# Performance work log

Hardware: AMD Instinct MI355X
Metric: run time of the kernel (lower is better)

Reference implementation:

```python
import jax, jax.numpy as jnp
import numpy as np

NUM_HEADS = 8
KEY_DIM = 256
EPS = 1e-16


def setup_inputs() -> dict:
    key = jax.random.key(0)
    k1, k2, k3, k4 = jax.random.split(key, 4)
    b, n, d, m = 2, 20000, 256, 320000
    q = jax.random.normal(k1, (b, n, d), dtype=jnp.float32)
    k = jax.random.normal(k2, (b, n, d), dtype=jnp.float32)
    e = jax.random.randint(k3, (2, m), 0, n, dtype=jnp.int64)
    r = jax.random.randint(k4, (m,), 0, n, dtype=jnp.int64)
    return {"q": q, "k": k, "e": e, "r": r}


def reference(q, k, e, r):
    b, n, d = q.shape
    m = e.shape[1]
    dh = d // NUM_HEADS
    # gather edge endpoints, multiply, sum within each head's d_head chunk
    # (scatter_sum over dim with h=[i//dh] == reshape + sum over last axis)
    src_q = q[:, e[0], :]                      # (b, m, d)
    dst_k = k[:, e[1], :]                      # (b, m, d)
    a = (src_q * dst_k).reshape(b, m, NUM_HEADS, dh).sum(-1)  # (b, m, H)
    a = a / jnp.sqrt(jnp.asarray(KEY_DIM, a.dtype))
    # segment softmax over edges grouped by r (global max subtraction, as in source)
    a = a - a.max()
    ex = jnp.exp(a)                            # (b, m, H)
    seg = jax.ops.segment_sum(ex.transpose(1, 0, 2), r, num_segments=n)  # (n, b, H)
    denom = seg[r].transpose(1, 0, 2)          # (b, m, H)
    return ex / (denom + EPS)
```

## Files before the change

kernel.cpp:

```cpp
#include <hip/hip_runtime.h>
#include <hip/hip_bf16.h>
#include <cmath>

#define D 256
#define NH 8
#define B 2
#define EPW 4
#define SSH 5
#define NBKMAX 1024
#define NCHMAX 512
#define SBLK 1024

#if defined(__has_builtin)
#  if __has_builtin(__builtin_amdgcn_fdot2_f32_bf16)
#    define USE_BF16_DOT 1
#  else
#    define USE_BF16_DOT 0
#  endif
#else
#  define USE_BF16_DOT 0
#endif

#if USE_BF16_DOT
typedef __bf16 bf16x2 __attribute__((ext_vector_type(2)));
#endif

__device__ inline unsigned short f2bf(float f) {
    unsigned u = __float_as_uint(f);
    unsigned r = u + 0x7FFFu + ((u >> 16) & 1u);
    return (unsigned short)(r >> 16);
}

__device__ inline float dot16(const uint4& a, const uint4& b) {
    float p = 0.f;
#if USE_BF16_DOT
    const bf16x2* av = (const bf16x2*)&a;
    const bf16x2* bv = (const bf16x2*)&b;
    #pragma unroll
    for (int w = 0; w < 4; ++w)
        p = __builtin_amdgcn_fdot2_f32_bf16(av[w], bv[w], p, false);
#else
    const unsigned* aw = (const unsigned*)&a;
    const unsigned* bw = (const unsigned*)&b;
    #pragma unroll
    for (int w = 0; w < 4; ++w) {
        float al = __uint_as_float(aw[w] << 16);
        float ah = __uint_as_float(aw[w] & 0xFFFF0000u);
        float bl = __uint_as_float(bw[w] << 16);
        float bh = __uint_as_float(bw[w] & 0xFFFF0000u);
        p = fmaf(al, bl, p);
        p = fmaf(ah, bh, p);
    }
#endif
    return p;
}

__global__ __launch_bounds__(256) void k_conv(
    const float* __restrict__ q, const float* __restrict__ k,
    uint4* __restrict__ qc, uint4* __restrict__ kc,
    float* __restrict__ seg, int segN, int n)
{
    int tid    = blockIdx.x * blockDim.x + threadIdx.x;
    int stride = gridDim.x * blockDim.x;
    for (int i = tid; i < segN; i += stride) seg[i] = 0.f;
    int total = n * B * 32;
    for (int i = tid; i < total; i += stride) {
        int c   = i & 31;
        int row = i >> 5;
        int bb  = (row >= n) ? 1 : 0;
        int node = row - bb * n;
        const float4* qs = (const float4*)(q + ((size_t)row << 8)) + (c << 1);
        const float4* ks = (const float4*)(k + ((size_t)row << 8)) + (c << 1);
        float4 a0 = qs[0], a1 = qs[1];
        float4 b0 = ks[0], b1 = ks[1];
        uint4 pa, pb;
        pa.x = (unsigned)f2bf(a0.x) | ((unsigned)f2bf(a0.y) << 16);
        pa.y = (unsigned)f2bf(a0.z) | ((unsigned)f2bf(a0.w) << 16);
        pa.z = (unsigned)f2bf(a1.x) | ((unsigned)f2bf(a1.y) << 16);
        pa.w = (unsigned)f2bf(a1.z) | ((unsigned)f2bf(a1.w) << 16);
        pb.x = (unsigned)f2bf(b0.x) | ((unsigned)f2bf(b0.y) << 16);
        pb.y = (unsigned)f2bf(b0.z) | ((unsigned)f2bf(b0.w) << 16);
        pb.z = (unsigned)f2bf(b1.x) | ((unsigned)f2bf(b1.y) << 16);
        pb.w = (unsigned)f2bf(b1.z) | ((unsigned)f2bf(b1.w) << 16);
        size_t dst = ((size_t)node * B + bb) * 32 + c;
        qc[dst] = pa;
        kc[dst] = pb;
    }
}


__global__ __launch_bounds__(256) void k_hist2(
    const int* __restrict__ e, int* __restrict__ bh, int m, int nbk)
{
    __shared__ int lh[NBKMAX];
    int b = blockIdx.x;
    int start = b * SBLK, end = min(m, start + SBLK);
    for (int t = threadIdx.x; t < nbk; t += 256) lh[t] = 0;
    __syncthreads();
    for (int j = start + threadIdx.x; j < end; j += 256)
        atomicAdd(&lh[e[j] >> SSH], 1);
    __syncthreads();
    for (int t = threadIdx.x; t < nbk; t += 256)
        bh[(size_t)b * nbk + t] = lh[t];
}

__global__ __launch_bounds__(NCHMAX) void k_colscan(
    int* __restrict__ bh, int* __restrict__ tot, int nch, int nbk)
{
    __shared__ int tmp[NCHMAX];
    int t = blockIdx.x;
    int b = threadIdx.x;
    int v = (b < nch) ? bh[(size_t)b * nbk + t] : 0;
    tmp[b] = v;
    __syncthreads();
    for (int off = 1; off < NCHMAX; off <<= 1) {
        int u = (b >= off) ? tmp[b - off] : 0;
        __syncthreads();
        tmp[b] += u;
        __syncthreads();
    }
    if (b < nch) bh[(size_t)b * nbk + t] = tmp[b] - v;
    if (b == NCHMAX - 1) tot[t] = tmp[b];
}

__global__ __launch_bounds__(256) void k_scatter2(
    const int* __restrict__ e, const int* __restrict__ r,
    const int* __restrict__ bh, const int* __restrict__ tot,
    int4* __restrict__ perm, int m, int nbk)
{
    __shared__ int tl[NBKMAX];
    __shared__ int tp[256];
    int b = blockIdx.x;
    int tid = threadIdx.x;
    for (int i = tid; i < NBKMAX; i += 256)
        tl[i] = (i < nbk) ? tot[i] : 0;
    __syncthreads();
    int s0 = tl[tid * 4 + 0], s1 = tl[tid * 4 + 1];
    int s2 = tl[tid * 4 + 2], s3 = tl[tid * 4 + 3];
    tl[tid * 4 + 0] = 0;
    tl[tid * 4 + 1] = s0;
    tl[tid * 4 + 2] = s0 + s1;
    tl[tid * 4 + 3] = s0 + s1 + s2;
    int v = s0 + s1 + s2 + s3;
    tp[tid] = v;
    __syncthreads();
    for (int off = 1; off < 256; off <<= 1) {
        int u = (tid >= off) ? tp[tid - off] : 0;
        __syncthreads();
        tp[tid] += u;
        __syncthreads();
    }
    int stripbase = tp[tid] - v;
    #pragma unroll
    for (int j2 = 0; j2 < 4; ++j2) tl[tid * 4 + j2] += stripbase;
    __syncthreads();
    __shared__ int cur[NBKMAX];
    for (int t = tid; t < nbk; t += 256)
        cur[t] = bh[(size_t)b * nbk + t] + tl[t];
    __syncthreads();
    int start = b * SBLK, end = min(m, start + SBLK);
    for (int j = start + tid; j < end; j += 256) {
        int e0 = e[j], e1 = e[m + j];
        int pos = atomicAdd(&cur[e0 >> SSH], 1);
        perm[pos] = make_int4(e0, e1, r[j], j);
    }
}

__global__ __launch_bounds__(256) void k_scores_perm(
    const ushort* __restrict__ qc, const ushort* __restrict__ kc,
    const int4* __restrict__ perm,
    float* __restrict__ s, float* __restrict__ seg, int m, int do_swz)
{
    int bid = blockIdx.x;
    if (do_swz) {
        int nb8 = gridDim.x >> 3;
        bid = (bid & 7) * nb8 + (bid >> 3);
    }
    int wave = (bid << 2) + (threadIdx.x >> 6);
    int lane = threadIdx.x & 63;
    int j0 = wave * EPW;
    if (j0 >= m) return;

    int rr[EPW], jo[EPW];
    uint4 qa[EPW], kb[EPW];
    #pragma unroll
    for (int t = 0; t < EPW; ++t) {
        int j = j0 + t;
        int4 p = (j < m) ? perm[j] : make_int4(0, 0, 0, -1);
        rr[t] = p.z;
        jo[t] = p.w;
        qa[t] = ((const uint4*)(qc + (size_t)p.x * (B * D)))[lane];
        kb[t] = ((const uint4*)(kc + (size_t)p.y * (B * D)))[lane];
    }
    __builtin_amdgcn_sched_barrier(0);

    #pragma unroll
    for (int t = 0; t < EPW; ++t) {
        float p = dot16(qa[t], kb[t]);
        p += __shfl_xor(p, 1);
        p += __shfl_xor(p, 2);
        float ex = __expf(p * 0.0625f);
        if ((lane & 3) == 0 && jo[t] >= 0) {
            int bb = lane >> 5;
            int h  = (lane >> 2) & 7;
            s[((size_t)bb * m + jo[t]) * NH + h] = ex;
            atomicAdd(&seg[((size_t)rr[t] * B + bb) * NH + h], ex);
        }
    }
}

__global__ __launch_bounds__(256) void k_scores_fused(
    const ushort* __restrict__ qc, const ushort* __restrict__ kc,
    const int* __restrict__ e, const int* __restrict__ r,
    float* __restrict__ s, float* __restrict__ seg, int m)
{
    int wave = (int)((blockIdx.x * blockDim.x + threadIdx.x) >> 6);
    int lane = threadIdx.x & 63;
    int j0 = wave * EPW;
    if (j0 >= m) return;

    int e0[EPW], e1[EPW], rr[EPW];
    #pragma unroll
    for (int t = 0; t < EPW; ++t) {
        int j = j0 + t;
        int ok = (j < m);
        e0[t] = ok ? e[j]     : 0;
        e1[t] = ok ? e[m + j] : 0;
        rr[t] = ok ? r[j]     : 0;
    }
    uint4 qa[EPW], kb[EPW];
    #pragma unroll
    for (int t = 0; t < EPW; ++t) {
        qa[t] = ((const uint4*)(qc + (size_t)e0[t] * (B * D)))[lane];
        kb[t] = ((const uint4*)(kc + (size_t)e1[t] * (B * D)))[lane];
    }
    __builtin_amdgcn_sched_barrier(0);
    #pragma unroll
    for (int t = 0; t < EPW; ++t) {
        float p = dot16(qa[t], kb[t]);
        p += __shfl_xor(p, 1);
        p += __shfl_xor(p, 2);
        float ex = __expf(p * 0.0625f);
        if ((lane & 3) == 0 && (j0 + t) < m) {
            int bb = lane >> 5;
            int h  = (lane >> 2) & 7;
            s[((size_t)bb * m + (j0 + t)) * NH + h] = ex;
            atomicAdd(&seg[((size_t)rr[t] * B + bb) * NH + h], ex);
        }
    }
}

__global__ __launch_bounds__(256) void k_scores_fused_f32(
    const float* __restrict__ q, const float* __restrict__ k,
    const int* __restrict__ e, const int* __restrict__ r,
    float* __restrict__ s, float* __restrict__ seg, int n, int m)
{
    int wave = (int)((blockIdx.x * blockDim.x + threadIdx.x) >> 6);
    int lane = threadIdx.x & 63;
    int j0 = wave * EPW;
    if (j0 >= m) return;
    int e0[EPW], e1[EPW], rr[EPW];
    #pragma unroll
    for (int t = 0; t < EPW; ++t) {
        int j = j0 + t; int ok = (j < m);
        e0[t] = ok ? e[j] : 0; e1[t] = ok ? e[m + j] : 0; rr[t] = ok ? r[j] : 0;
    }
    float4 qa[B][EPW], kb[B][EPW];
    #pragma unroll
    for (int bb = 0; bb < B; ++bb)
        #pragma unroll
        for (int t = 0; t < EPW; ++t) {
            qa[bb][t] = ((const float4*)(q + ((size_t)bb * n + e0[t]) * D))[lane];
            kb[bb][t] = ((const float4*)(k + ((size_t)bb * n + e1[t]) * D))[lane];
        }
    #pragma unroll
    for (int bb = 0; bb < B; ++bb)
        #pragma unroll
        for (int t = 0; t < EPW; ++t) {
            float4 A = qa[bb][t], K4 = kb[bb][t];
            float p = A.x * K4.x + A.y * K4.y + A.z * K4.z + A.w * K4.w;
            p += __shfl_xor(p, 1); p += __shfl_xor(p, 2); p += __shfl_xor(p, 4);
            float ex = __expf(p * 0.0625f);
            if ((lane & 7) == 0 && (j0 + t) < m) {
                int h = lane >> 3;
                s[((size_t)bb * m + (j0 + t)) * NH + h] = ex;
                atomicAdd(&seg[((size_t)rr[t] * B + bb) * NH + h], ex);
            }
        }
}

__global__ __launch_bounds__(256) void k_norm(
    float* __restrict__ s, const int* __restrict__ r,
    const float* __restrict__ seg, int m)
{
    int i = blockIdx.x * blockDim.x + threadIdx.x;
    int total = B * m;
    if (i >= total) return;
    int bb = (i >= m) ? 1 : 0;
    int j  = i - bb * m;
    const float4* sg = (const float4*)(seg + ((size_t)r[j] * B + bb) * NH);
    float4* sp = (float4*)(s + (size_t)i * NH);
    float4 d0 = sg[0], d1 = sg[1];
    float4 x0 = sp[0], x1 = sp[1];
    x0.x = __fdividef(x0.x, d0.x + 1e-16f);
    x0.y = __fdividef(x0.y, d0.y + 1e-16f);
    x0.z = __fdividef(x0.z, d0.z + 1e-16f);
    x0.w = __fdividef(x0.w, d0.w + 1e-16f);
    x1.x = __fdividef(x1.x, d1.x + 1e-16f);
    x1.y = __fdividef(x1.y, d1.y + 1e-16f);
    x1.z = __fdividef(x1.z, d1.z + 1e-16f);
    x1.w = __fdividef(x1.w, d1.w + 1e-16f);
    sp[0] = x0; sp[1] = x1;
}

extern "C" void kernel_launch(void* const* d_in, const int* in_sizes, int n_in,
                              void* d_out, int out_size, void* d_ws, size_t ws_size,
                              hipStream_t stream) {
    const float* q = (const float*)d_in[0];
    const float* k = (const float*)d_in[1];
    const int*   e = (const int*)d_in[2];
    const int*   r = (const int*)d_in[3];
    float* s = (float*)d_out;

    int n = in_sizes[0] / (B * D);
    int m = in_sizes[3];
    int nbk  = (n + (1 << SSH) - 1) >> SSH;
    int nch  = (m + SBLK - 1) / SBLK;
    int segN = n * B * NH;

    size_t seg_bytes  = (size_t)segN * sizeof(float);
    size_t row_bytes  = (size_t)n * B * D * sizeof(unsigned short);
    size_t perm_bytes = (size_t)m * sizeof(int4);
    size_t bh_bytes   = (size_t)nch * nbk * sizeof(int);
    size_t tb_bytes   = NBKMAX * sizeof(int);

    float*  seg  = (float*)d_ws;
    ushort* qc   = (ushort*)((char*)d_ws + seg_bytes);
    ushort* kc   = (ushort*)((char*)d_ws + seg_bytes + row_bytes);
    int4*   perm = (int4*)((char*)d_ws + seg_bytes + 2 * row_bytes);
    int*    bh   = (int*)((char*)d_ws + seg_bytes + 2 * row_bytes + perm_bytes);
    int*    tot  = (int*)((char*)bh + bh_bytes);

    bool use_bf16 = ws_size >= (seg_bytes + 2 * row_bytes);
    bool use_sort = use_bf16 && nbk <= NBKMAX && nch <= NCHMAX &&
                    ws_size >= (seg_bytes + 2 * row_bytes + perm_bytes +
                                bh_bytes + tb_bytes);

    int nblocks = (B * m + 255) / 256;
    int nwaves  = (m + EPW - 1) / EPW;
    int sblocks = (nwaves + 3) / 4;

    if (use_bf16) {
        int cblocks = (n * B * 32 + 255) / 256;
        k_conv<<<cblocks, 256, 0, stream>>>(q, k, (uint4*)qc, (uint4*)kc,
                                            seg, segN, n);
        if (use_sort) {
            k_hist2<<<nch, 256, 0, stream>>>(e, bh, m, nbk);
            k_colscan<<<nbk, NCHMAX, 0, stream>>>(bh, tot, nch, nbk);
            k_scatter2<<<nch, 256, 0, stream>>>(e, r, bh, tot, perm, m, nbk);
            int do_swz = (sblocks % 8 == 0) ? 1 : 0;
            k_scores_perm<<<sblocks, 256, 0, stream>>>(qc, kc, perm, s, seg, m, do_swz);
        } else {
            k_scores_fused<<<sblocks, 256, 0, stream>>>(qc, kc, e, r, s, seg, m);
        }
    } else {
        hipMemsetAsync(d_ws, 0, seg_bytes, stream);
        k_scores_fused_f32<<<sblocks, 256, 0, stream>>>(q, k, e, r, s, seg, n, m);
    }
    k_norm<<<nblocks, 256, 0, stream>>>(s, r, seg, m);
}
```

Before: 207.1 us.

## Subsort bucketed edges by exact source node and share q row loads

Adds a second-pass kernel that sorts each source-node bucket (32 nodes) by the low bits of the source index in shared memory, so edges sharing a source become adjacent. The scores kernel then checks whether all four edges of a wave have the same source and, if so, loads the q row once instead of four times. This is meant to cut gather traffic for q rows, at the cost of an extra kernel launch and an extra read/write pass over the permutation array. With about 16 edges per source, many groups of four may share a source, but the uniformity check adds a branch.

New measurement: 214.2 us. +3.4%, slower.

```diff
diff --git a/kernel.cpp b/kernel.cpp
--- a/kernel.cpp
+++ b/kernel.cpp
@@ -10,6 +10,7 @@
 #define NBKMAX 1024
 #define NCHMAX 512
 #define SBLK 1024
+#define SUBCAP 2048
 
 #if defined(__has_builtin)
 #  if __has_builtin(__builtin_amdgcn_fdot2_f32_bf16)
@@ -126,7 +127,7 @@
 __global__ __launch_bounds__(256) void k_scatter2(
     const int* __restrict__ e, const int* __restrict__ r,
     const int* __restrict__ bh, const int* __restrict__ tot,
-    int4* __restrict__ perm, int m, int nbk)
+    int4* __restrict__ perm, int* __restrict__ baseout, int m, int nbk)
 {
     __shared__ int tl[NBKMAX];
     __shared__ int tp[256];
@@ -154,6 +155,8 @@
     #pragma unroll
     for (int j2 = 0; j2 < 4; ++j2) tl[tid * 4 + j2] += stripbase;
     __syncthreads();
+    if (b == 0)
+        for (int t = tid; t < nbk; t += 256) baseout[t] = tl[t];
     __shared__ int cur[NBKMAX];
     for (int t = tid; t < nbk; t += 256)
         cur[t] = bh[(size_t)b * nbk + t] + tl[t];
@@ -166,6 +169,34 @@
     }
 }
 
+__global__ __launch_bounds__(256) void k_subsort(
+    int4* __restrict__ perm, const int* __restrict__ base, int m, int nbk)
+{
+    __shared__ int4 buf[SUBCAP];
+    __shared__ int hist[64], off[64];
+    int t = blockIdx.x;
+    int start = base[t];
+    int end   = (t + 1 < nbk) ? base[t + 1] : m;
+    int len   = end - start;
+    if (len <= 1 || len > SUBCAP) return;
+    for (int i = threadIdx.x; i < len; i += 256) buf[i] = perm[start + i];
+    if (threadIdx.x < 64) hist[threadIdx.x] = 0;
+    __syncthreads();
+    for (int i = threadIdx.x; i < len; i += 256)
+        atomicAdd(&hist[buf[i].x & 63], 1);
+    __syncthreads();
+    if (threadIdx.x == 0) {
+        int run = 0;
+        #pragma unroll
+        for (int i = 0; i < 64; ++i) { off[i] = run; run += hist[i]; }
+    }
+    __syncthreads();
+    for (int i = threadIdx.x; i < len; i += 256) {
+        int pos = atomicAdd(&off[buf[i].x & 63], 1);
+        perm[start + pos] = buf[i];
+    }
+}
+
 __global__ __launch_bounds__(256) void k_scores_perm(
     const ushort* __restrict__ qc, const ushort* __restrict__ kc,
     const int4* __restrict__ perm,
@@ -181,16 +212,31 @@
     int j0 = wave * EPW;
     if (j0 >= m) return;
 
-    int rr[EPW], jo[EPW];
-    uint4 qa[EPW], kb[EPW];
+    int rr[EPW], jo[EPW], e0s[EPW], e1s[EPW];
     #pragma unroll
     for (int t = 0; t < EPW; ++t) {
         int j = j0 + t;
         int4 p = (j < m) ? perm[j] : make_int4(0, 0, 0, -1);
-        rr[t] = p.z;
-        jo[t] = p.w;
-        qa[t] = ((const uint4*)(qc + (size_t)p.x * (B * D)))[lane];
-        kb[t] = ((const uint4*)(kc + (size_t)p.y * (B * D)))[lane];
+        e0s[t] = p.x;
+        e1s[t] = p.y;
+        rr[t]  = p.z;
+        jo[t]  = p.w;
+    }
+
+    uint4 qa[EPW], kb[EPW];
+    bool uni = (e0s[0] == e0s[1]) & (e0s[1] == e0s[2]) & (e0s[2] == e0s[3]);
+    if (uni) {
+        qa[0] = ((const uint4*)(qc + (size_t)e0s[0] * (B * D)))[lane];
+        #pragma unroll
+        for (int t = 0; t < EPW; ++t)
+            kb[t] = ((const uint4*)(kc + (size_t)e1s[t] * (B * D)))[lane];
+        qa[1] = qa[0]; qa[2] = qa[0]; qa[3] = qa[0];
+    } else {
+        #pragma unroll
+        for (int t = 0; t < EPW; ++t) {
+            qa[t] = ((const uint4*)(qc + (size_t)e0s[t] * (B * D)))[lane];
+            kb[t] = ((const uint4*)(kc + (size_t)e1s[t] * (B * D)))[lane];
+        }
     }
     __builtin_amdgcn_sched_barrier(0);
 
@@ -332,7 +378,7 @@
     size_t row_bytes  = (size_t)n * B * D * sizeof(unsigned short);
     size_t perm_bytes = (size_t)m * sizeof(int4);
     size_t bh_bytes   = (size_t)nch * nbk * sizeof(int);
-    size_t tb_bytes   = NBKMAX * sizeof(int);
+    size_t tb_bytes   = 2 * NBKMAX * sizeof(int);
 
     float*  seg  = (float*)d_ws;
     ushort* qc   = (ushort*)((char*)d_ws + seg_bytes);
@@ -340,6 +386,7 @@
     int4*   perm = (int4*)((char*)d_ws + seg_bytes + 2 * row_bytes);
     int*    bh   = (int*)((char*)d_ws + seg_bytes + 2 * row_bytes + perm_bytes);
     int*    tot  = (int*)((char*)bh + bh_bytes);
+    int*    base = tot + NBKMAX;
 
     bool use_bf16 = ws_size >= (seg_bytes + 2 * row_bytes);
     bool use_sort = use_bf16 && nbk <= NBKMAX && nch <= NCHMAX &&
@@ -357,7 +404,8 @@
         if (use_sort) {
             k_hist2<<<nch, 256, 0, stream>>>(e, bh, m, nbk);
             k_colscan<<<nbk, NCHMAX, 0, stream>>>(bh, tot, nch, nbk);
-            k_scatter2<<<nch, 256, 0, stream>>>(e, r, bh, tot, perm, m, nbk);
+            k_scatter2<<<nch, 256, 0, stream>>>(e, r, bh, tot, perm, base, m, nbk);
+            k_subsort<<<nbk, 256, 0, stream>>>(perm, base, m, nbk);
             int do_swz = (sblocks % 8 == 0) ? 1 : 0;
             k_scores_perm<<<sblocks, 256, 0, stream>>>(qc, kc, perm, s, seg, m, do_swz);
         } else {
```
